# Optimization experiments

Measured on AMD Instinct MI355X. Metric: run time of the kernel, lower is better.

Reference implementation:

```python
import jax, jax.numpy as jnp
import numpy as np

EPS = 1e-5

def group_norm(x, gamma, beta, groups=32):
    # x: [B, C, S, K]; GroupNorm over (C//groups, S, K) per group
    B, C = x.shape[0], x.shape[1]
    sp = x.shape[2:]
    xg = x.reshape(B, groups, C // groups, -1)
    mu = xg.mean(axis=(2, 3), keepdims=True)
    var = xg.var(axis=(2, 3), keepdims=True)
    xg = (xg - mu) / jnp.sqrt(var + EPS)
    xo = xg.reshape(B, C, *sp)
    bshape = (1, C) + (1,) * len(sp)
    return xo * gamma.reshape(bshape) + beta.reshape(bshape)

def leaky(x, slope):
    return jnp.where(x >= 0, x, slope * x)

def setup_inputs() -> dict:
    key = jax.random.key(0)
    ks = jax.random.split(key, 12)
    B, C, P, S = 4, 4, 16384, 8192
    x = jax.random.normal(ks[0], (B, C, P), dtype=jnp.float32)
    # random sampling permutation (done inside torch forward; externalized for determinism)
    perm = jax.vmap(lambda k: jax.random.permutation(k, P)[:S])(jax.random.split(ks[1], B)).astype(jnp.int32)
    sc = 0.1
    return {
        "x": x,
        "perm": perm,
        "num_points": S,
        "pos_w": jax.random.normal(ks[2], (32, 10), dtype=jnp.float32) * sc,
        "bn2_g": jnp.ones((32,), jnp.float32),
        "bn2_b": jnp.zeros((32,), jnp.float32),
        "conv_w": jax.random.normal(ks[3], (32, 4), dtype=jnp.float32) * sc,
        "bn_g": jnp.ones((32,), jnp.float32),
        "bn_b": jnp.zeros((32,), jnp.float32),
        "att_w1": jax.random.normal(ks[4], (32, 64), dtype=jnp.float32) * sc,
        "att_w2": jax.random.normal(ks[5], (1, 32), dtype=jnp.float32) * sc,
        "b1_w": jax.random.normal(ks[6], (64, 64), dtype=jnp.float32) * sc,
        "b2_w": jax.random.normal(ks[7], (64, 4), dtype=jnp.float32) * sc,
    }

def reference(x, perm, num_points, pos_w, bn2_g, bn2_b, conv_w, bn_g, bn_b, att_w1, att_w2, b1_w, b2_w):
    B, C, P = x.shape
    S = num_points
    K = 16  # neighb
    # Dynamic_sampling: gather sampled points
    sel = jnp.take_along_axis(x, jnp.broadcast_to(perm[:, None, :], (B, C, S)).astype(jnp.int32), axis=2)  # [B,C,S]
    # knn on xyz (torch.no_grad)
    xs = jax.lax.stop_gradient(x[:, :3, :])
    ss = jax.lax.stop_gradient(sel[:, :3, :])
    pd = (2.0 * jnp.einsum('bcp,bcs->bps', xs, ss)
          - jnp.sum(xs * xs, axis=1)[:, :, None]
          - jnp.sum(ss * ss, axis=1)[:, None, :])  # [B,P,S] = -dist^2
    _, idx = jax.lax.top_k(jnp.transpose(pd, (0, 2, 1)), K)  # [B,S,K] (== torch idx [B,K,S] transposed)
    # torch quirk: idx [B,K,S] flattened then viewed as (B,S,K)
    idx_q = jnp.transpose(idx, (0, 2, 1)).reshape(B, S, K)
    x_t = jnp.transpose(x, (0, 2, 1))  # [B,P,C]
    feat = x_t[jnp.arange(B)[:, None, None], idx_q]  # [B,S,K,C]
    x1 = jnp.transpose(feat, (0, 3, 1, 2))  # [B,C,S,K]
    # positional encoding
    PA = x1[:, :3, :, :]                    # [B,3,S,K]
    PC = x1[:, :3, :, :1]                   # [B,3,S,1] center
    d = PA - PC
    temp = jnp.sqrt(jnp.sum(d * d, axis=1, keepdims=True))  # [B,1,S,K]
    PEmb = jnp.concatenate([PA, jnp.broadcast_to(PC, PA.shape), d, temp], axis=1)  # [B,10,S,K]
    pe = leaky(group_norm(jnp.einsum('oc,bcsk->bosk', pos_w, PEmb), bn2_g, bn2_b), 0.2)
    xc = leaky(group_norm(jnp.einsum('oc,bcsk->bosk', conv_w, x1), bn_g, bn_b), 0.2)  # C==4 branch
    feature = jnp.concatenate([xc, pe], axis=1)  # [B,64,S,K]
    att = jnp.einsum('oc,bcsk->bosk', att_w2, leaky(jnp.einsum('oc,bcsk->bosk', att_w1, feature), 0.2))  # [B,1,S,K]
    att = jax.nn.softmax(att, axis=-1)
    pooled = jnp.sum(feature * att, axis=-1)  # [B,64,S]
    Fea1 = jnp.einsum('oc,bcs->bos', b1_w, pooled)
    Fea2 = jnp.einsum('oc,bcs->bos', b2_w, x1[:, :, :, 0])  # C==4 branch
    out = leaky(Fea1 + Fea2, 0.1)
    return jnp.concatenate([x1[:, :4, :, 0], out], axis=1)  # [B,68,S]
```

## Files before the change

kernel.cpp:

```cpp
#include <hip/hip_runtime.h>
#include <math.h>

#define DEVI static __device__ __forceinline__

constexpr int Bn = 4, Cn = 4, Pn = 16384, Sn = 8192, Kn = 16;
constexpr float GN_N = 131072.0f;
constexpr int PART_STRIDE = 96;
constexpr int ST_CHUNKS = 256;
constexpr int GD = 16;
constexpr int NCELL = GD * GD * GD;
constexpr float BND = 5.5f;
constexpr float CH = 0.6875f;
constexpr float INVH = 1.4545455f;
constexpr float SLACK = 1e-3f;

DEVI float mulrn(float a, float b){ return __fmul_rn(a, b); }
DEVI float addrn(float a, float b){ return __fadd_rn(a, b); }
DEVI float subrn(float a, float b){ return __fsub_rn(a, b); }
DEVI float leaky(float v, float s){ return v >= 0.0f ? v : s * v; }

DEVI int clampi(int v, int lo, int hi){ return v < lo ? lo : (v > hi ? hi : v); }

DEVI float dpp_up1f(float x){
  int xi = __builtin_bit_cast(int, x);
  int r = __builtin_amdgcn_update_dpp(xi, xi, 0x111, 0xF, 0xF, false);
  return __builtin_bit_cast(float, r);
}
DEVI int dpp_up1i(int x){
  return __builtin_amdgcn_update_dpp(x, x, 0x111, 0xF, 0xF, false);
}
DEVI float swz15(float x){
  int xi = __builtin_bit_cast(int, x);
  int r = __builtin_amdgcn_ds_swizzle(xi, 0x1FF);
  return __builtin_bit_cast(float, r);
}
DEVI int swz15i(int x){ return __builtin_amdgcn_ds_swizzle(x, 0x1FF); }

DEVI int cellof(float4 v, int &cx, int &cy, int &cz){
  cx = clampi((int)((v.x + BND) * INVH), 0, GD - 1);
  cy = clampi((int)((v.y + BND) * INVH), 0, GD - 1);
  cz = clampi((int)((v.z + BND) * INVH), 0, GD - 1);
  return (cx * GD + cy) * GD + cz;
}

DEVI float cm1(float q, int c){
  float lo = -BND + c * CH, hi = lo + CH;
  float d = 0.f;
  if (c > 0      && q < lo) d = lo - q;
  if (c < GD - 1 && q > hi) d = q - hi;
  return d * d;
}

__global__ void k_pack(const float* __restrict__ x, float4* __restrict__ pk,
                       int* __restrict__ hist){
  int i = blockIdx.x * 256 + threadIdx.x;
  int b = i >> 14, p = i & (Pn - 1);
  const float* xb = x + (size_t)b * Cn * Pn;
  float x0 = xb[p], x1 = xb[Pn + p], x2 = xb[2 * Pn + p];
  float n = addrn(addrn(mulrn(x0, x0), mulrn(x1, x1)), mulrn(x2, x2));
  pk[i] = make_float4(x0, x1, x2, n);
  if (i < Bn * 2 * NCELL) hist[i] = 0;
}

__global__ void k_hist(const float4* __restrict__ pk, const int* __restrict__ perm,
                       int* __restrict__ hist){
  int i = blockIdx.x * 256 + threadIdx.x;
  int b = i >> 14;
  int cx, cy, cz;
  int c = cellof(pk[i], cx, cy, cz);
  atomicAdd(&hist[b * NCELL + c], 1);
  if (i < Bn * Sn){
    int b2 = i >> 13;
    int q = perm[i];
    int c2 = cellof(pk[b2 * Pn + q], cx, cy, cz);
    atomicAdd(&hist[(4 + b2) * NCELL + c2], 1);
  }
}

__launch_bounds__(1024)
__global__ void k_scan(const int* __restrict__ hist, int* __restrict__ cellstart,
                       int* __restrict__ cursor){
  __shared__ int sh[1024];
  const int u = blockIdx.x, t = threadIdx.x;
  const int base = u * NCELL + t * 4;
  int sum = 0;
#pragma unroll
  for (int i = 0; i < 4; ++i) sum += hist[base + i];
  sh[t] = sum;
  __syncthreads();
  for (int off = 1; off < 1024; off <<= 1){
    int v = (t >= off) ? sh[t - off] : 0;
    __syncthreads();
    sh[t] += v;
    __syncthreads();
  }
  int run = sh[t] - sum;
  const int cbase = u * (NCELL + 1) + t * 4;
#pragma unroll
  for (int i = 0; i < 4; ++i){
    cellstart[cbase + i] = run;
    cursor[cbase + i] = run;
    run += hist[base + i];
  }
  if (t == 1023) cellstart[u * (NCELL + 1) + NCELL] = run;
}

__global__ void k_scatter(const float4* __restrict__ pk, const int* __restrict__ perm,
                          int* __restrict__ cursor, float4* __restrict__ spt,
                          int* __restrict__ sid, int* __restrict__ qord){
  int i = blockIdx.x * 256 + threadIdx.x;
  int b = i >> 14, p = i & (Pn - 1);
  float4 v = pk[i];
  int cx, cy, cz;
  int c = cellof(v, cx, cy, cz);
  int slot = atomicAdd(&cursor[b * (NCELL + 1) + c], 1);
  spt[b * Pn + slot] = v;
  sid[b * Pn + slot] = p;
  if (i < Bn * Sn){
    int b2 = i >> 13, s = i & (Sn - 1);
    int q = perm[i];
    int c2 = cellof(pk[b2 * Pn + q], cx, cy, cz);
    int slot2 = atomicAdd(&cursor[(4 + b2) * (NCELL + 1) + c2], 1);
    qord[b2 * Sn + slot2] = s;
  }
}

#define VISITC(CX, CY, CZ, BXY)                                               \
  { const float m2_ = (BXY) + cm1(qz, (CZ));                                  \
    if (!(t15 > -1e37f) || -m2_ >= t15 - SLACK){                              \
      const int c_ = ((CX) * GD + (CY)) * GD + (CZ);                          \
      const int j0_ = lcs[c_], j1_ = lcs[c_ + 1];                             \
      for (int j = j0_ + lane16; j - lane16 < j1_; j += 16){                  \
        float cpd = -INFINITY; int cpi = 0x7FFFFFFF;                          \
        if (j < j1_){                                                         \
          const float4 v = spt[pb + j];                                       \
          const float dot = addrn(addrn(mulrn(v.x, qx), mulrn(v.y, qy)),      \
                                  mulrn(v.z, qz));                            \
          cpd = subrn(subrn(mulrn(2.0f, dot), v.w), qw);                      \
          cpi = sid[pb + j];                                                  \
        }                                                                     \
        const unsigned long long m0 =                                         \
          __ballot((cpd > t15) || (cpd == t15 && cpi < i15)) & gmask;         \
        unsigned long long mm = m0;                                           \
        while (mm){                                                           \
          const int src = __builtin_ctzll(mm);                                \
          mm &= mm - 1;                                                       \
          const float cv = __shfl(cpd, src);                                  \
          const int   ci = __shfl(cpi, src);                                  \
          const float upv = dpp_up1f(lv);                                     \
          const int   upi = dpp_up1i(li);                                     \
          const bool keep = (lv > cv) || (lv == cv && li < ci);               \
          const bool ins  = (!keep) &&                                        \
            (lane0 || (upv > cv) || (upv == cv && upi < ci));                 \
          lv = keep ? lv : (ins ? cv : upv);                                  \
          li = keep ? li : (ins ? ci : upi);                                  \
        }                                                                     \
        if (m0){ t15 = swz15(lv); i15 = swz15i(li); }                         \
      }                                                                       \
    } }

__launch_bounds__(256)
__global__ void k_topk(const float4* __restrict__ pk, const float4* __restrict__ spt,
                       const int* __restrict__ sid, const int* __restrict__ cellstart,
                       const int* __restrict__ perm, const int* __restrict__ qord,
                       int* __restrict__ idx){
  __shared__ int lcs[NCELL + 1];
  const int b = blockIdx.y;
  const int tid = threadIdx.x;
  const int lane = tid & 63;
  const int lane16 = lane & 15;
  const bool lane0 = (lane16 == 0);
  const int g = lane >> 4;
  const unsigned long long gmask = 0xFFFFull << (g * 16);
  const int s = qord[b * Sn + blockIdx.x * 16 + (tid >> 4)];

  const int cb = b * (NCELL + 1);
  for (int j = tid; j <= NCELL; j += 256) lcs[j] = cellstart[cb + j];

  const int q = perm[b * Sn + s];
  const float4 sv = pk[b * Pn + q];
  const float qx = sv.x, qy = sv.y, qz = sv.z, qw = sv.w;
  int qcx, qcy, qcz;
  cellof(sv, qcx, qcy, qcz);
  const int pb = b * Pn;
  __syncthreads();

  float lv = -INFINITY;  int li = 0x7FFFFFFF;
  float t15 = -INFINITY; int i15 = 0x7FFFFFFF;

  for (int r = 0; r < GD; ++r){
    if (r >= 1 && t15 > -1e37f){
      const float lb = (float)(r - 1) * CH;
      if (-(lb * lb) < t15 - SLACK) break;
    }
    const int x0 = clampi(qcx - r, 0, GD - 1), x1 = clampi(qcx + r, 0, GD - 1);
    const int y0 = clampi(qcy - r, 0, GD - 1), y1 = clampi(qcy + r, 0, GD - 1);
    for (int cx = x0; cx <= x1; ++cx){
      const int adx = cx > qcx ? cx - qcx : qcx - cx;
      const float bx = cm1(qx, cx);
      for (int cy = y0; cy <= y1; ++cy){
        const int ady = cy > qcy ? cy - qcy : qcy - cy;
        const float bxy = bx + cm1(qy, cy);
        if ((t15 > -1e37f) && -bxy < t15 - SLACK) continue;
        if (adx == r || ady == r){
          const int z0c = clampi(qcz - r, 0, GD - 1);
          const int z1c = clampi(qcz + r, 0, GD - 1);
          const int colb = (cx * GD + cy) * GD;
          if (lcs[colb + z0c] == lcs[colb + z1c + 1]) continue;
          for (int cz = z0c; cz <= z1c; ++cz) VISITC(cx, cy, cz, bxy)
        } else {
          int cz = qcz - r;
          if (cz >= 0) VISITC(cx, cy, cz, bxy)
          cz = qcz + r;
          if (cz <= GD - 1) VISITC(cx, cy, cz, bxy)
        }
      }
    }
  }

  idx[((size_t)(b * Sn + s)) * Kn + lane16] = li;
}
#undef VISITC

DEVI int idxq(const int* __restrict__ idxb, int f){
  return idxb[(f & (Sn - 1)) * Kn + (f >> 13)];
}

DEVI float wred(float v){
  v += __shfl_down(v, 32); v += __shfl_down(v, 16); v += __shfl_down(v, 8);
  v += __shfl_down(v, 4);  v += __shfl_down(v, 2);  v += __shfl_down(v, 1);
  return v;
}

__global__ void k_stats(const float4* __restrict__ pk, const float* __restrict__ x,
                        const int* __restrict__ idx, float* __restrict__ part){
  const int b = blockIdx.y, chunk = blockIdx.x, tid = threadIdx.x;
  const int sp = chunk * 32 + (tid >> 3);
  const int kq = tid & 7;
  const int* idxb = idx + b * Sn * Kn;
  const float* xw = x + ((size_t)b * Cn + 3) * Pn;

  float M10[55], mu10[10], M4[10], mu4[4];
#pragma unroll
  for (int i = 0; i < 55; ++i) M10[i] = 0.f;
#pragma unroll
  for (int i = 0; i < 10; ++i){ mu10[i] = 0.f; M4[i] = 0.f; }
#pragma unroll
  for (int i = 0; i < 4; ++i) mu4[i] = 0.f;

  const int qc = idxq(idxb, sp * 16);
  const float4 cv = pk[b * Pn + qc];

#pragma unroll
  for (int kk = 0; kk < 2; ++kk){
    const int k = kq * 2 + kk;
    const int qn = idxq(idxb, sp * 16 + k);
    const float4 pv = pk[b * Pn + qn];
    const float pw = xw[qn];
    const float dx = subrn(pv.x, cv.x), dy = subrn(pv.y, cv.y), dz = subrn(pv.z, cv.z);
    const float temp = sqrtf(addrn(addrn(mulrn(dx, dx), mulrn(dy, dy)), mulrn(dz, dz)));
    const float E[10] = {pv.x, pv.y, pv.z, cv.x, cv.y, cv.z, dx, dy, dz, temp};
    const float X[4]  = {pv.x, pv.y, pv.z, pw};
    int c = 0;
#pragma unroll
    for (int i = 0; i < 10; ++i){
      mu10[i] += E[i];
#pragma unroll
      for (int j = i; j < 10; ++j){ M10[c] += E[i] * E[j]; ++c; }
    }
    c = 0;
#pragma unroll
    for (int i = 0; i < 4; ++i){
      mu4[i] += X[i];
#pragma unroll
      for (int j = i; j < 4; ++j){ M4[c] += X[i] * X[j]; ++c; }
    }
  }

  __shared__ float red[4][80];
  const int wid = tid >> 6, ln = tid & 63;
#pragma unroll
  for (int i = 0; i < 55; ++i){ float v = wred(M10[i]); if (ln == 0) red[wid][i] = v; }
#pragma unroll
  for (int i = 0; i < 10; ++i){ float v = wred(mu10[i]); if (ln == 0) red[wid][55 + i] = v; }
#pragma unroll
  for (int i = 0; i < 10; ++i){ float v = wred(M4[i]); if (ln == 0) red[wid][65 + i] = v; }
#pragma unroll
  for (int i = 0; i < 4; ++i){ float v = wred(mu4[i]); if (ln == 0) red[wid][75 + i] = v; }
  __syncthreads();
  if (tid < 79){
    float sum = ((red[0][tid] + red[1][tid]) + red[2][tid]) + red[3][tid];
    part[(b * ST_CHUNKS + chunk) * PART_STRIDE + tid] = sum;
  }
}

__global__ void k_stats2(const float* __restrict__ part,
                         const float* __restrict__ pos_w, const float* __restrict__ conv_w,
                         const float* __restrict__ bn2_g, const float* __restrict__ bn2_b,
                         const float* __restrict__ bn_g,  const float* __restrict__ bn_b,
                         float2* __restrict__ stats){
  __shared__ float phalf[8][80];
  __shared__ float sacc[4][80];
  const int t = threadIdx.x;
  if (t < 640){
    const int pair = t / 80, i = t % 80;
    if (i < 79){
      const int bb = pair >> 1, half = pair & 1;
      float a = 0.f;
      for (int c = half * 128; c < half * 128 + 128; ++c)
        a += part[(bb * ST_CHUNKS + c) * PART_STRIDE + i];
      phalf[pair][i] = a;
    }
  }
  __syncthreads();
  if (t < 320){
    const int bb = t / 80, i = t % 80;
    if (i < 79) sacc[bb][i] = phalf[bb * 2][i] + phalf[bb * 2 + 1][i];
  }
  __syncthreads();
  if (t >= 256) return;
  const int b = t >> 6, o = t & 63;
  const float* acc = sacc[b];
  float mean, ex2, gamma, beta;
  if (o < 32){
    const float* w = conv_w + o * 4;
    float m = 0.f, e2 = 0.f; int id = 0;
#pragma unroll
    for (int i = 0; i < 4; ++i){
      m += w[i] * acc[75 + i];
#pragma unroll
      for (int j = i; j < 4; ++j){
        float t2 = w[i] * w[j] * acc[65 + id];
        e2 += (i == j) ? t2 : 2.0f * t2; ++id;
      }
    }
    mean = m / GN_N; ex2 = e2 / GN_N; gamma = bn_g[o]; beta = bn_b[o];
  } else {
    const float* w = pos_w + (o - 32) * 10;
    float m = 0.f, e2 = 0.f; int id = 0;
#pragma unroll
    for (int i = 0; i < 10; ++i){
      m += w[i] * acc[55 + i];
#pragma unroll
      for (int j = i; j < 10; ++j){
        float t2 = w[i] * w[j] * acc[id];
        e2 += (i == j) ? t2 : 2.0f * t2; ++id;
      }
    }
    mean = m / GN_N; ex2 = e2 / GN_N; gamma = bn2_g[o - 32]; beta = bn2_b[o - 32];
  }
  const float var = fmaxf(ex2 - mean * mean, 0.f);
  const float rstd = 1.0f / sqrtf(var + 1e-5f);
  const float scale = rstd * gamma;
  stats[b * 64 + o] = make_float2(scale, beta - mean * scale);
}

__global__ void k_final(const float4* __restrict__ pk, const float* __restrict__ x,
                        const int* __restrict__ idx, const float2* __restrict__ stats,
                        const float* __restrict__ conv_w, const float* __restrict__ pos_w,
                        const float* __restrict__ att_w1, const float* __restrict__ att_w2,
                        const float* __restrict__ b1_w, const float* __restrict__ b2_w,
                        float* __restrict__ out){
  __shared__ float ob[68][17];
  const int b = blockIdx.y;
  const int tid = threadIdx.x;
  const int k = tid & 15;
  const int spl = tid >> 4;
  const int sp0 = blockIdx.x * 16;
  const int sp = sp0 + spl;
  const int* idxb = idx + b * Sn * Kn;
  const float* xw = x + ((size_t)b * Cn + 3) * Pn;

  const int qn = idxq(idxb, sp * 16 + k);
  const float4 pv = pk[b * Pn + qn];
  const float pw = xw[qn];
  const float cx = __shfl(pv.x, 0, 16), cy = __shfl(pv.y, 0, 16);
  const float cz = __shfl(pv.z, 0, 16), cw = __shfl(pw, 0, 16);
  const float dx = subrn(pv.x, cx), dy = subrn(pv.y, cy), dz = subrn(pv.z, cz);
  const float temp = sqrtf(addrn(addrn(mulrn(dx, dx), mulrn(dy, dy)), mulrn(dz, dz)));
  const float E[10]  = {pv.x, pv.y, pv.z, cx, cy, cz, dx, dy, dz, temp};
  const float X4[4]  = {pv.x, pv.y, pv.z, pw};
  const float2* stb = stats + b * 64;

  float feat[64];
  for (int o = 0; o < 32; ++o){
    float v = 0.f;
#pragma unroll
    for (int c = 0; c < 4; ++c) v = fmaf(conv_w[o * 4 + c], X4[c], v);
    const float2 sc = stb[o];
    feat[o] = leaky(fmaf(v, sc.x, sc.y), 0.2f);
  }
  for (int o = 0; o < 32; ++o){
    float v = 0.f;
#pragma unroll
    for (int c = 0; c < 10; ++c) v = fmaf(pos_w[o * 10 + c], E[c], v);
    const float2 sc = stb[32 + o];
    feat[32 + o] = leaky(fmaf(v, sc.x, sc.y), 0.2f);
  }

  float logit = 0.f;
  for (int h = 0; h < 32; ++h){
    float v = 0.f;
#pragma unroll
    for (int c = 0; c < 64; ++c) v = fmaf(att_w1[h * 64 + c], feat[c], v);
    logit = fmaf(att_w2[h], leaky(v, 0.2f), logit);
  }
  float mx = logit;
  mx = fmaxf(mx, __shfl_xor(mx, 1, 16)); mx = fmaxf(mx, __shfl_xor(mx, 2, 16));
  mx = fmaxf(mx, __shfl_xor(mx, 4, 16)); mx = fmaxf(mx, __shfl_xor(mx, 8, 16));
  const float e = expf(logit - mx);
  float den = e;
  den += __shfl_xor(den, 1, 16); den += __shfl_xor(den, 2, 16);
  den += __shfl_xor(den, 4, 16); den += __shfl_xor(den, 8, 16);
  const float att = e / den;

#pragma unroll
  for (int c = 0; c < 64; ++c){
    float p = feat[c] * att;
    p += __shfl_xor(p, 1, 16); p += __shfl_xor(p, 2, 16);
    p += __shfl_xor(p, 4, 16); p += __shfl_xor(p, 8, 16);
    feat[c] = p;
  }

  const float X0[4] = {cx, cy, cz, cw};
#pragma unroll
  for (int jj = 0; jj < 4; ++jj){
    const int j = k * 4 + jj;
    float f1 = 0.f;
#pragma unroll
    for (int c = 0; c < 64; ++c) f1 = fmaf(b1_w[j * 64 + c], feat[c], f1);
    float f2 = 0.f;
#pragma unroll
    for (int c = 0; c < 4; ++c) f2 = fmaf(b2_w[j * 4 + c], X0[c], f2);
    ob[4 + j][spl] = leaky(f1 + f2, 0.1f);
  }
  if (k == 0){
    ob[0][spl] = cx; ob[1][spl] = cy; ob[2][spl] = cz; ob[3][spl] = cw;
  }
  __syncthreads();
  float* outb = out + (size_t)b * 68 * Sn;
  for (int e2 = tid; e2 < 68 * 16; e2 += 256){
    const int r = e2 >> 4, c = e2 & 15;
    outb[(size_t)r * Sn + sp0 + c] = ob[r][c];
  }
}

extern "C" void kernel_launch(void* const* d_in, const int* in_sizes, int n_in,
                              void* d_out, int out_size, void* d_ws, size_t ws_size,
                              hipStream_t stream){
  const float* x      = (const float*)d_in[0];
  const int*   perm   = (const int*)d_in[1];
  const float* pos_w  = (const float*)d_in[3];
  const float* bn2_g  = (const float*)d_in[4];
  const float* bn2_b  = (const float*)d_in[5];
  const float* conv_w = (const float*)d_in[6];
  const float* bn_g   = (const float*)d_in[7];
  const float* bn_b   = (const float*)d_in[8];
  const float* att_w1 = (const float*)d_in[9];
  const float* att_w2 = (const float*)d_in[10];
  const float* b1_w   = (const float*)d_in[11];
  const float* b2_w   = (const float*)d_in[12];
  float* out = (float*)d_out;

  char* ws = (char*)d_ws;
  int*    idx       = (int*)ws;
  float4* pk        = (float4*)(ws + 2097152);
  float4* spt       = (float4*)(ws + 3145728);
  int*    sid       = (int*)(ws + 4194304);
  int*    hist      = (int*)(ws + 4456448);
  int*    cellstart = (int*)(ws + 4587520);
  int*    cursor    = (int*)(ws + 4718848);
  int*    qord      = (int*)(ws + 4850176);
  float*  part      = (float*)(ws + 4981248);
  float2* stats     = (float2*)(ws + 5374464);

  hipLaunchKernelGGL(k_pack,    dim3(256),          dim3(256),  0, stream, x, pk, hist);
  hipLaunchKernelGGL(k_hist,    dim3(256),          dim3(256),  0, stream, pk, perm, hist);
  hipLaunchKernelGGL(k_scan,    dim3(8),            dim3(1024), 0, stream, hist,
                     cellstart, cursor);
  hipLaunchKernelGGL(k_scatter, dim3(256),          dim3(256),  0, stream, pk, perm,
                     cursor, spt, sid, qord);
  hipLaunchKernelGGL(k_topk,    dim3(512, 4),       dim3(256),  0, stream, pk, spt, sid,
                     cellstart, perm, qord, idx);
  hipLaunchKernelGGL(k_stats,   dim3(ST_CHUNKS, 4), dim3(256),  0, stream, pk, x, idx, part);
  hipLaunchKernelGGL(k_stats2,  dim3(1),            dim3(640),  0, stream, part, pos_w, conv_w,
                     bn2_g, bn2_b, bn_g, bn_b, stats);
  hipLaunchKernelGGL(k_final,   dim3(512, 4),       dim3(256),  0, stream, pk, x, idx, stats,
                     conv_w, pos_w, att_w1, att_w2, b1_w, b2_w, out);
}
```

Measured before the change: 275.9 us.

## Fuse histogram into pack, prefetch kNN candidates, merge small z-column ranges

Folds the histogram pass into the pack kernel and zeroes the histogram with a memset, removing one launch. Query cell coordinates are now computed directly from x instead of from the packed buffer. In the kNN top-k kernel, candidate loads are software-prefetched one 16-wide batch ahead, and contiguous z-column cell ranges with at most 32 points are scanned as one range instead of cell by cell. The trade-off is higher register use, the loss of per-cell pruning inside the small merged columns, and an extra memset node.

```diff
diff --git a/kernel.cpp b/kernel.cpp
--- a/kernel.cpp
+++ b/kernel.cpp
@@ -51,28 +51,23 @@
   return d * d;
 }
 
-__global__ void k_pack(const float* __restrict__ x, float4* __restrict__ pk,
-                       int* __restrict__ hist){
+__global__ void k_pack(const float* __restrict__ x, const int* __restrict__ perm,
+                       float4* __restrict__ pk, int* __restrict__ hist){
   int i = blockIdx.x * 256 + threadIdx.x;
   int b = i >> 14, p = i & (Pn - 1);
   const float* xb = x + (size_t)b * Cn * Pn;
   float x0 = xb[p], x1 = xb[Pn + p], x2 = xb[2 * Pn + p];
   float n = addrn(addrn(mulrn(x0, x0), mulrn(x1, x1)), mulrn(x2, x2));
   pk[i] = make_float4(x0, x1, x2, n);
-  if (i < Bn * 2 * NCELL) hist[i] = 0;
-}
-
-__global__ void k_hist(const float4* __restrict__ pk, const int* __restrict__ perm,
-                       int* __restrict__ hist){
-  int i = blockIdx.x * 256 + threadIdx.x;
-  int b = i >> 14;
   int cx, cy, cz;
-  int c = cellof(pk[i], cx, cy, cz);
+  int c = cellof(make_float4(x0, x1, x2, n), cx, cy, cz);
   atomicAdd(&hist[b * NCELL + c], 1);
   if (i < Bn * Sn){
     int b2 = i >> 13;
     int q = perm[i];
-    int c2 = cellof(pk[b2 * Pn + q], cx, cy, cz);
+    const float* xb2 = x + (size_t)b2 * Cn * Pn;
+    float4 qv = make_float4(xb2[q], xb2[Pn + q], xb2[2 * Pn + q], 0.f);
+    int c2 = cellof(qv, cx, cy, cz);
     atomicAdd(&hist[(4 + b2) * NCELL + c2], 1);
   }
 }
@@ -125,38 +120,40 @@
   }
 }
 
-#define VISITC(CX, CY, CZ, BXY)                                               \
-  { const float m2_ = (BXY) + cm1(qz, (CZ));                                  \
-    if (!(t15 > -1e37f) || -m2_ >= t15 - SLACK){                              \
-      const int c_ = ((CX) * GD + (CY)) * GD + (CZ);                          \
-      const int j0_ = lcs[c_], j1_ = lcs[c_ + 1];                             \
-      for (int j = j0_ + lane16; j - lane16 < j1_; j += 16){                  \
-        float cpd = -INFINITY; int cpi = 0x7FFFFFFF;                          \
-        if (j < j1_){                                                         \
-          const float4 v = spt[pb + j];                                       \
-          const float dot = addrn(addrn(mulrn(v.x, qx), mulrn(v.y, qy)),      \
-                                  mulrn(v.z, qz));                            \
-          cpd = subrn(subrn(mulrn(2.0f, dot), v.w), qw);                      \
-          cpi = sid[pb + j];                                                  \
-        }                                                                     \
-        const unsigned long long m0 =                                         \
-          __ballot((cpd > t15) || (cpd == t15 && cpi < i15)) & gmask;         \
-        unsigned long long mm = m0;                                           \
-        while (mm){                                                           \
-          const int src = __builtin_ctzll(mm);                                \
-          mm &= mm - 1;                                                       \
-          const float cv = __shfl(cpd, src);                                  \
-          const int   ci = __shfl(cpi, src);                                  \
-          const float upv = dpp_up1f(lv);                                     \
-          const int   upi = dpp_up1i(li);                                     \
-          const bool keep = (lv > cv) || (lv == cv && li < ci);               \
-          const bool ins  = (!keep) &&                                        \
-            (lane0 || (upv > cv) || (upv == cv && upi < ci));                 \
-          lv = keep ? lv : (ins ? cv : upv);                                  \
-          li = keep ? li : (ins ? ci : upi);                                  \
-        }                                                                     \
-        if (m0){ t15 = swz15(lv); i15 = swz15i(li); }                         \
+#define RSCAN(J0, J1)                                                         \
+  { int jb_ = (J0); const int je_ = (J1);                                     \
+    float4 pv_; int pidx_;                                                    \
+    bool pok_ = jb_ + lane16 < je_;                                           \
+    if (pok_){ pv_ = spt[pb + jb_ + lane16]; pidx_ = sid[pb + jb_ + lane16]; }\
+    for (; jb_ < je_; jb_ += 16){                                             \
+      const float4 v = pv_; const int pi = pidx_; const bool ok = pok_;       \
+      const int jn_ = jb_ + 16 + lane16;                                      \
+      pok_ = jn_ < je_;                                                       \
+      if (pok_){ pv_ = spt[pb + jn_]; pidx_ = sid[pb + jn_]; }                \
+      float cpd = -INFINITY; int cpi = 0x7FFFFFFF;                            \
+      if (ok){                                                                \
+        const float dot = addrn(addrn(mulrn(v.x, qx), mulrn(v.y, qy)),        \
+                                mulrn(v.z, qz));                              \
+        cpd = subrn(subrn(mulrn(2.0f, dot), v.w), qw);                        \
+        cpi = pi;                                                             \
       }                                                                       \
+      const unsigned long long m0 =                                           \
+        __ballot((cpd > t15) || (cpd == t15 && cpi < i15)) & gmask;           \
+      unsigned long long mm = m0;                                             \
+      while (mm){                                                             \
+        const int src = __builtin_ctzll(mm);                                  \
+        mm &= mm - 1;                                                         \
+        const float cv = __shfl(cpd, src);                                    \
+        const int   ci = __shfl(cpi, src);                                    \
+        const float upv = dpp_up1f(lv);                                       \
+        const int   upi = dpp_up1i(li);                                       \
+        const bool keep = (lv > cv) || (lv == cv && li < ci);                 \
+        const bool ins  = (!keep) &&                                          \
+          (lane0 || (upv > cv) || (upv == cv && upi < ci));                   \
+        lv = keep ? lv : (ins ? cv : upv);                                    \
+        li = keep ? li : (ins ? ci : upi);                                    \
+      }                                                                       \
+      if (m0){ t15 = swz15(lv); i15 = swz15i(li); }                           \
     } }
 
 __launch_bounds__(256)
@@ -202,17 +199,39 @@
         const int ady = cy > qcy ? cy - qcy : qcy - cy;
         const float bxy = bx + cm1(qy, cy);
         if ((t15 > -1e37f) && -bxy < t15 - SLACK) continue;
+        const int colb = (cx * GD + cy) * GD;
         if (adx == r || ady == r){
           const int z0c = clampi(qcz - r, 0, GD - 1);
           const int z1c = clampi(qcz + r, 0, GD - 1);
-          const int colb = (cx * GD + cy) * GD;
-          if (lcs[colb + z0c] == lcs[colb + z1c + 1]) continue;
-          for (int cz = z0c; cz <= z1c; ++cz) VISITC(cx, cy, cz, bxy)
+          const int cj0 = lcs[colb + z0c], cj1 = lcs[colb + z1c + 1];
+          if (cj0 == cj1) continue;
+          if (cj1 - cj0 <= 32){
+            RSCAN(cj0, cj1)
+          } else {
+            for (int cz = z0c; cz <= z1c; ++cz){
+              const float m2_ = bxy + cm1(qz, cz);
+              if ((t15 > -1e37f) && -m2_ < t15 - SLACK) continue;
+              const int c_ = colb + cz;
+              RSCAN(lcs[c_], lcs[c_ + 1])
+            }
+          }
         } else {
           int cz = qcz - r;
-          if (cz >= 0) VISITC(cx, cy, cz, bxy)
+          if (cz >= 0){
+            const float m2_ = bxy + cm1(qz, cz);
+            if (!((t15 > -1e37f) && -m2_ < t15 - SLACK)){
+              const int c_ = colb + cz;
+              RSCAN(lcs[c_], lcs[c_ + 1])
+            }
+          }
           cz = qcz + r;
-          if (cz <= GD - 1) VISITC(cx, cy, cz, bxy)
+          if (cz <= GD - 1){
+            const float m2_ = bxy + cm1(qz, cz);
+            if (!((t15 > -1e37f) && -m2_ < t15 - SLACK)){
+              const int c_ = colb + cz;
+              RSCAN(lcs[c_], lcs[c_ + 1])
+            }
+          }
         }
       }
     }
@@ -220,7 +239,7 @@
 
   idx[((size_t)(b * Sn + s)) * Kn + lane16] = li;
 }
-#undef VISITC
+#undef RSCAN
 
 DEVI int idxq(const int* __restrict__ idxb, int f){
   return idxb[(f & (Sn - 1)) * Kn + (f >> 13)];
@@ -474,8 +493,8 @@
   float*  part      = (float*)(ws + 4981248);
   float2* stats     = (float2*)(ws + 5374464);
 
-  hipLaunchKernelGGL(k_pack,    dim3(256),          dim3(256),  0, stream, x, pk, hist);
-  hipLaunchKernelGGL(k_hist,    dim3(256),          dim3(256),  0, stream, pk, perm, hist);
+  hipMemsetAsync(hist, 0, Bn * 2 * NCELL * sizeof(int), stream);
+  hipLaunchKernelGGL(k_pack,    dim3(256),          dim3(256),  0, stream, x, perm, pk, hist);
   hipLaunchKernelGGL(k_scan,    dim3(8),            dim3(1024), 0, stream, hist,
                      cellstart, cursor);
   hipLaunchKernelGGL(k_scatter, dim3(256),          dim3(256),  0, stream, pk, perm,
```

Result: slower. 283.6 us (+2.8%).
